# Kernel tuning notes

Measured on AMD Instinct MI355X. Metric: run time of the kernel, lower is better.

Reference implementation:

```python
import jax, jax.numpy as jnp
import numpy as np

B, T, H, L, OUT = 64, 2048, 256, 2, 256


def setup_inputs() -> dict:
    key = jax.random.key(0)
    ks = jax.random.split(key, 7)
    s = 1.0 / np.sqrt(H)
    return {
        "x": jax.random.normal(ks[0], (B, T, H), dtype=jnp.float32),
        "W_ih": jax.random.uniform(ks[1], (L, 4 * H, H), jnp.float32, -s, s),
        "W_hh": jax.random.uniform(ks[2], (L, 4 * H, H), jnp.float32, -s, s),
        "b_ih": jax.random.uniform(ks[3], (L, 4 * H), jnp.float32, -s, s),
        "b_hh": jax.random.uniform(ks[4], (L, 4 * H), jnp.float32, -s, s),
        "W_fc": jax.random.uniform(ks[5], (OUT, H), jnp.float32, -s, s),
        "b_fc": jax.random.uniform(ks[6], (OUT,), jnp.float32, -s, s),
    }


def _lstm_forward(x, W_ih, W_hh, b_ih, b_hh, W_fc, b_fc):
    n_layers = W_ih.shape[0]
    batch = x.shape[0]
    hidden = W_hh.shape[2]
    h0 = jnp.zeros((n_layers, batch, hidden), x.dtype)
    c0 = jnp.zeros((n_layers, batch, hidden), x.dtype)

    def step(carry, x_t):
        h, c = carry  # [L, B, H] each
        inp = x_t  # [B, in]
        new_h, new_c = [], []
        for l in range(n_layers):
            # gates: [B, 4H] = x W_ih^T + b_ih + h W_hh^T + b_hh
            gates = (inp @ W_ih[l].T + b_ih[l]) + (h[l] @ W_hh[l].T + b_hh[l])
            i_g, f_g, g_g, o_g = jnp.split(gates, 4, axis=-1)
            c_new = jax.nn.sigmoid(f_g) * c[l] + jax.nn.sigmoid(i_g) * jnp.tanh(g_g)
            h_new = jax.nn.sigmoid(o_g) * jnp.tanh(c_new)
            new_h.append(h_new)
            new_c.append(c_new)
            inp = h_new
        return (jnp.stack(new_h), jnp.stack(new_c)), None

    (h_T, _), _ = jax.lax.scan(step, (h0, c0), jnp.swapaxes(x, 0, 1))
    # fc applied to last timestep's top-layer hidden state
    return h_T[-1] @ W_fc.T + b_fc  # [B, OUT]


def reference(x, W_ih, W_hh, b_ih, b_hh, W_fc, b_fc):
    return _lstm_forward(x, W_ih, W_hh, b_ih, b_hh, W_fc, b_fc)
```

## Files before the change

### kernel.cpp

```cpp
#include <hip/hip_runtime.h>
#include <math.h>

typedef unsigned long long u64;
typedef __attribute__((ext_vector_type(8))) short short8v;
typedef __attribute__((ext_vector_type(4))) float f32x4;

#define LB 64
#define LT 2048
#define LH 256
#define LOUT 256
#define NWG 256

#define WS_CNT    0
#define WS_CNT_SZ ((size_t)8 * 32 * 16 * sizeof(int))
#define WS_H1     (64 * 1024)
#define WS_H2     (WS_H1 + 256 * 1024)
#define WS_BIAS   (WS_H2 + 256 * 1024)
#define WS_WT2    (1024 * 1024)
#define HSLOT     8192

#define MFMA(a, b, c) __builtin_amdgcn_mfma_f32_16x16x32_bf16(a, b, c, 0, 0, 0)
#define LD_IC(p) __hip_atomic_load((p), __ATOMIC_RELAXED, __HIP_MEMORY_SCOPE_AGENT)
#define ST_IC(p, v) __hip_atomic_store((p), (v), __ATOMIC_RELAXED, __HIP_MEMORY_SCOPE_AGENT)

__device__ __host__ __forceinline__ short bf16_rne(float f) {
    unsigned u = __builtin_bit_cast(unsigned, f);
    unsigned r = (u + 0x7fffu + ((u >> 16) & 1u)) >> 16;
    return (short)r;
}
__device__ __forceinline__ float bf16_to_f(short s) {
    unsigned u = ((unsigned)(unsigned short)s) << 16;
    return __builtin_bit_cast(float, u);
}
__device__ __forceinline__ float fsigm(float g) {
    return __builtin_amdgcn_rcpf(1.f + __builtin_amdgcn_exp2f(g * -1.44269504f));
}
__device__ __forceinline__ float ftanh(float g) {
    return __builtin_amdgcn_rcpf(1.f + __builtin_amdgcn_exp2f(g * -2.88539008f)) * 2.f - 1.f;
}

__global__ void prep_weights(const float* __restrict__ W_ih,
                             const float* __restrict__ W_hh,
                             const float* __restrict__ b_ih,
                             const float* __restrict__ b_hh,
                             unsigned short* __restrict__ Wt2,
                             float* __restrict__ bias_r) {
    int gid = blockIdx.x * 256 + threadIdx.x;
    if (gid >= (1 << 20)) return;
    int j   = gid & 7;
    int rwi = (gid >> 3) & 15;
    int kgi = (gid >> 7) & 3;
    int ks  = (gid >> 9) & 15;
    int mt  = (gid >> 13) & 3;
    int s   = (gid >> 15) & 15;
    int layer = gid >> 19;
    int k   = ks * 32 + kgi * 8 + j;
    int row = mt * 256 + s * 16 + rwi;
    float w = (k < 256) ? W_ih[((size_t)layer * 1024 + row) * 256 + k]
                        : W_hh[((size_t)layer * 1024 + row) * 256 + (k - 256)];
    short hi = bf16_rne(w);
    float rem = w - bf16_to_f(hi);
    short lo = bf16_rne(rem);
    size_t base = (((size_t)((layer * 16 + s) * 4 + mt) * 16 + ks) * 1024)
                  + (size_t)kgi * 128 + rwi * 8 + j;
    Wt2[base]       = (unsigned short)hi;
    Wt2[base + 512] = (unsigned short)lo;
    if (k == 0) {
        int ridx = s * 64 + mt * 16 + rwi;
        bias_r[layer * 1024 + ridx] = b_ih[layer * 1024 + row] + b_hh[layer * 1024 + row];
    }
}

__global__ __launch_bounds__(256, 1)
void lstm_persistent(const float* __restrict__ x,
                     const unsigned short* __restrict__ Wt2,
                     const float* __restrict__ bias_r,
                     u64* __restrict__ h1, u64* __restrict__ h2,
                     int* __restrict__ cnt)
{
    __shared__ __align__(16) f32x4 red[12][64];

    const int tid   = threadIdx.x;
    const int wg    = blockIdx.x;
    const int layer = wg >> 7;
    const int g     = wg & 127;
    const int bg    = g & 7;
    const int s     = g >> 3;
    const int b0    = bg * 8;
    const int wave  = tid >> 6;
    const int lane  = tid & 63;
    const int kg    = lane >> 4;
    const int rw    = lane & 15;
    const int rb    = rw & 7;
    const int batch = b0 + rb;
    int* const fl_base = cnt + (size_t)bg * 32 * 16;
    const int  myflag  = (layer * 16 + s) * 16;

    short8v Ahi[4][4], Alo[4][4];
    #pragma unroll
    for (int mt = 0; mt < 4; ++mt)
        #pragma unroll
        for (int k2 = 0; k2 < 4; ++k2) {
            size_t base = (((size_t)((layer * 16 + s) * 4 + mt) * 16 + (wave * 4 + k2)) * 1024)
                          + (size_t)kg * 128 + rw * 8;
            Ahi[mt][k2] = *(const short8v*)((const short*)Wt2 + base);
            Alo[mt][k2] = *(const short8v*)((const short*)Wt2 + base + 512);
        }

    f32x4 biasv[4];
    #pragma unroll
    for (int mt = 0; mt < 4; ++mt)
        biasv[mt] = *(const f32x4*)(bias_r + layer * 1024 + s * 64 + mt * 16 + kg * 4);

    f32x4 creg = {0.f, 0.f, 0.f, 0.f};

    float4 xr[4][2];
    if (layer == 0 && wave < 2) {
        #pragma unroll
        for (int k2 = 0; k2 < 4; ++k2) {
            const int kbase = (wave * 4 + k2) * 32 + kg * 8;
            const float* xp = x + ((size_t)batch * LT + 0) * LH + kbase;
            xr[k2][0] = *(const float4*)xp;
            xr[k2][1] = *(const float4*)(xp + 4);
        }
    }

    for (int r = 0; r <= LT; ++r) {
        const bool active = (layer == 0) ? (r < LT) : (r >= 1);
        const int t = (layer == 0) ? r : (r - 1);

        short8v Bhi[4], Blo[4];
        bool useB = false;
        if (active) {
            if (layer == 0 && wave < 2) {
                #pragma unroll
                for (int k2 = 0; k2 < 4; ++k2) {
                    float fv[8] = {xr[k2][0].x, xr[k2][0].y, xr[k2][0].z, xr[k2][0].w,
                                   xr[k2][1].x, xr[k2][1].y, xr[k2][1].z, xr[k2][1].w};
                    short8v bh, bl;
                    #pragma unroll
                    for (int j = 0; j < 8; ++j) {
                        short hb = bf16_rne(fv[j]);
                        bh[j] = hb;
                        bl[j] = bf16_rne(fv[j] - bf16_to_f(hb));
                    }
                    Bhi[k2] = bh; Blo[k2] = bl;
                }
                useB = true;
            } else {
                const u64* hb; size_t slotbase; int kofs; bool any;
                if (layer == 0) {
                    any = (t > 0); hb = h1; slotbase = (size_t)((t - 1) & 3) * HSLOT; kofs = -256;
                } else if (wave < 2) {
                    any = true;    hb = h1; slotbase = (size_t)(t & 3) * HSLOT; kofs = 0;
                } else {
                    any = (t > 0); hb = h2; slotbase = (size_t)((t - 1) & 3) * HSLOT; kofs = -256;
                }
                if (any) {
                    u64 q[4][4];
                    #pragma unroll
                    for (int k2 = 0; k2 < 4; ++k2) {
                        const int kbase = (wave * 4 + k2) * 32 + kg * 8 + kofs;
                        size_t qi = slotbase + (size_t)batch * 128 + (kbase >> 2) * 2;
                        q[k2][0] = LD_IC(hb + qi);
                        q[k2][1] = LD_IC(hb + qi + 1);
                        q[k2][2] = LD_IC(hb + qi + 2);
                        q[k2][3] = LD_IC(hb + qi + 3);
                    }
                    #pragma unroll
                    for (int k2 = 0; k2 < 4; ++k2) {
                        union { u64 qq[2]; short8v v; } ch, cl;
                        ch.qq[0] = q[k2][0]; ch.qq[1] = q[k2][2];
                        cl.qq[0] = q[k2][1]; cl.qq[1] = q[k2][3];
                        Bhi[k2] = ch.v; Blo[k2] = cl.v;
                    }
                    useB = true;
                }
            }
        }

        f32x4 acc[4];
        #pragma unroll
        for (int mt = 0; mt < 4; ++mt) acc[mt] = (f32x4){0.f, 0.f, 0.f, 0.f};
        if (useB) {
            #pragma unroll
            for (int k2 = 0; k2 < 4; ++k2)
                #pragma unroll
                for (int mt = 0; mt < 4; ++mt) {
                    acc[mt] = MFMA(Ahi[mt][k2], Bhi[k2], acc[mt]);
                    acc[mt] = MFMA(Ahi[mt][k2], Blo[k2], acc[mt]);
                    acc[mt] = MFMA(Alo[mt][k2], Bhi[k2], acc[mt]);
                }
        }

        if (active && wave > 0) {
            #pragma unroll
            for (int mt = 0; mt < 4; ++mt) red[(wave - 1) * 4 + mt][lane] = acc[mt];
        }
        __syncthreads();

        if (active && wave == 0) {
            f32x4 gate[4];
            #pragma unroll
            for (int mt = 0; mt < 4; ++mt) {
                f32x4 gs = acc[mt] + biasv[mt];
                #pragma unroll
                for (int w = 0; w < 3; ++w) gs += red[w * 4 + mt][lane];
                gate[mt] = gs;
            }
            float hv[4];
            #pragma unroll
            for (int rr = 0; rr < 4; ++rr) {
                float si = fsigm(gate[0][rr]);
                float sf = fsigm(gate[1][rr]);
                float so = fsigm(gate[3][rr]);
                float gg = ftanh(gate[2][rr]);
                float cn = sf * creg[rr] + si * gg;
                creg[rr] = cn;
                hv[rr] = so * ftanh(cn);
            }
            if (rw < 8) {
                u64 qh = 0, ql = 0;
                #pragma unroll
                for (int rr = 0; rr < 4; ++rr) {
                    short hb = bf16_rne(hv[rr]);
                    short lb = bf16_rne(hv[rr] - bf16_to_f(hb));
                    qh |= ((u64)(unsigned short)hb) << (16 * rr);
                    ql |= ((u64)(unsigned short)lb) << (16 * rr);
                }
                u64* dst = (layer == 0 ? h1 : h2);
                size_t qi = (size_t)(t & 3) * HSLOT + (size_t)(b0 + rw) * 128 + (s * 4 + kg) * 2;
                ST_IC(dst + qi, qh);
                ST_IC(dst + qi + 1, ql);
            }
        }

        if (wave == 0 && r < LT) {
            asm volatile("s_waitcnt vmcnt(0)" ::: "memory");
            if (lane == 0) ST_IC(fl_base + myflag, r + 1);
        }

        if (layer == 0 && wave < 2 && t + 1 < LT) {
            #pragma unroll
            for (int k2 = 0; k2 < 4; ++k2) {
                const int kbase = (wave * 4 + k2) * 32 + kg * 8;
                const float* xp = x + ((size_t)batch * LT + (t + 1)) * LH + kbase;
                xr[k2][0] = *(const float4*)xp;
                xr[k2][1] = *(const float4*)(xp + 4);
            }
        }

        if (r < LT) {
            if (wave == 0) {
                const int mL = lane >> 4;
                const int tgt = (layer == 0) ? ((mL == 0) ? r + 1 : r - 1) : (r + 1);
                const int* fp = fl_base + (size_t)(lane & 31) * 16;
                for (;;) {
                    int v = (lane < 32) ? LD_IC(fp) : 0x7fffffff;
                    if (__all(v >= tgt)) break;
                    __builtin_amdgcn_s_sleep(1);
                }
            }
            __syncthreads();
        }
    }
}

__global__ __launch_bounds__(256)
void fc_kernel(const u64* __restrict__ h2w,
               const float* __restrict__ W_fc,
               const float* __restrict__ b_fc,
               float* __restrict__ out) {
    int b = blockIdx.x;
    int o = threadIdx.x;
    __shared__ float hrow[LH];
    for (int k = threadIdx.x; k < LH; k += 256) {
        size_t w = (size_t)3 * HSLOT + (size_t)b * 128 + (k >> 2) * 2;
        int sh = (k & 3) * 16;
        short hi = (short)((h2w[w]     >> sh) & 0xffff);
        short lo = (short)((h2w[w + 1] >> sh) & 0xffff);
        hrow[k] = bf16_to_f(hi) + bf16_to_f(lo);
    }
    __syncthreads();
    float acc = b_fc[o];
#pragma unroll 8
    for (int k = 0; k < LH; ++k)
        acc = fmaf(W_fc[o * LH + k], hrow[k], acc);
    out[b * LOUT + o] = acc;
}

extern "C" void kernel_launch(void* const* d_in, const int* in_sizes, int n_in,
                              void* d_out, int out_size, void* d_ws, size_t ws_size,
                              hipStream_t stream) {
    const float* x    = (const float*)d_in[0];
    const float* W_ih = (const float*)d_in[1];
    const float* W_hh = (const float*)d_in[2];
    const float* b_ih = (const float*)d_in[3];
    const float* b_hh = (const float*)d_in[4];
    const float* W_fc = (const float*)d_in[5];
    const float* b_fc = (const float*)d_in[6];
    float* out = (float*)d_out;

    char* ws = (char*)d_ws;
    int*            cnt    = (int*)(ws + WS_CNT);
    u64*            h1     = (u64*)(ws + WS_H1);
    u64*            h2     = (u64*)(ws + WS_H2);
    float*          bias_r = (float*)(ws + WS_BIAS);
    unsigned short* Wt2    = (unsigned short*)(ws + WS_WT2);

    hipMemsetAsync(cnt, 0, WS_CNT_SZ, stream);
    prep_weights<<<(1 << 20) / 256, 256, 0, stream>>>(W_ih, W_hh, b_ih, b_hh, Wt2, bias_r);

    void* args[] = {(void*)&x, (void*)&Wt2, (void*)&bias_r,
                    (void*)&h1, (void*)&h2, (void*)&cnt};
    hipError_t e = hipLaunchCooperativeKernel(lstm_persistent, dim3(NWG), dim3(256),
                                              args, 0, stream);
    if (e != hipSuccess) {
        lstm_persistent<<<NWG, 256, 0, stream>>>(x, Wt2, bias_r, h1, h2, cnt);
    }

    fc_kernel<<<LB, 256, 0, stream>>>(h2, W_fc, b_fc, out);
}
```

Before: 8.513 ms.

## Embed parity tags in hidden-state data to replace flag-based inter-WG barriers

Removes the per-step flag barrier and __syncthreads wait. Consumers now poll the hidden-state data itself: a parity bit tied to the step is stored in the LSB of each low bf16 word, and data is written and read as 16-byte units with system-coherent loads and stores. Only a slim backpressure flag from layer 1 to layer 0 remains, and the LDS reduction buffer is double-buffered so consecutive steps do not race. This cuts synchronization latency on the recurrent critical path, at the cost of one bit of precision in the low correction term and relying on 16-byte store atomicity.

```diff
diff --git a/kernel.cpp b/kernel.cpp
--- a/kernel.cpp
+++ b/kernel.cpp
@@ -4,6 +4,7 @@
 typedef unsigned long long u64;
 typedef __attribute__((ext_vector_type(8))) short short8v;
 typedef __attribute__((ext_vector_type(4))) float f32x4;
+typedef __attribute__((ext_vector_type(4))) unsigned uint4v;
 
 #define LB 64
 #define LT 2048
@@ -12,12 +13,12 @@
 #define NWG 256
 
 #define WS_CNT    0
-#define WS_CNT_SZ ((size_t)8 * 32 * 16 * sizeof(int))
+#define WS_CNT_SZ ((size_t)8 * 16 * 16 * sizeof(int))
 #define WS_H1     (64 * 1024)
 #define WS_H2     (WS_H1 + 256 * 1024)
 #define WS_BIAS   (WS_H2 + 256 * 1024)
 #define WS_WT2    (1024 * 1024)
-#define HSLOT     8192
+#define HBYTES    (256 * 1024)
 
 #define MFMA(a, b, c) __builtin_amdgcn_mfma_f32_16x16x32_bf16(a, b, c, 0, 0, 0)
 #define LD_IC(p) __hip_atomic_load((p), __ATOMIC_RELAXED, __HIP_MEMORY_SCOPE_AGENT)
@@ -75,10 +76,10 @@
 void lstm_persistent(const float* __restrict__ x,
                      const unsigned short* __restrict__ Wt2,
                      const float* __restrict__ bias_r,
-                     u64* __restrict__ h1, u64* __restrict__ h2,
+                     char* __restrict__ h1c, char* __restrict__ h2c,
                      int* __restrict__ cnt)
 {
-    __shared__ __align__(16) f32x4 red[12][64];
+    __shared__ __align__(16) f32x4 red[2][12][64];
 
     const int tid   = threadIdx.x;
     const int wg    = blockIdx.x;
@@ -93,8 +94,7 @@
     const int rw    = lane & 15;
     const int rb    = rw & 7;
     const int batch = b0 + rb;
-    int* const fl_base = cnt + (size_t)bg * 32 * 16;
-    const int  myflag  = (layer * 16 + s) * 16;
+    int* const flags = cnt + bg * 256;
 
     short8v Ahi[4][4], Alo[4][4];
     #pragma unroll
@@ -148,32 +148,58 @@
                 }
                 useB = true;
             } else {
-                const u64* hb; size_t slotbase; int kofs; bool any;
-                if (layer == 0) {
-                    any = (t > 0); hb = h1; slotbase = (size_t)((t - 1) & 3) * HSLOT; kofs = -256;
-                } else if (wave < 2) {
-                    any = true;    hb = h1; slotbase = (size_t)(t & 3) * HSLOT; kofs = 0;
-                } else {
-                    any = (t > 0); hb = h2; slotbase = (size_t)((t - 1) & 3) * HSLOT; kofs = -256;
-                }
+                const char* hbuf; int slot, kofs, tg; bool any;
+                if (layer == 0)      { any = (t > 0); hbuf = h1c; slot = (t - 1) & 3; kofs = -256; tg = ((t - 1) >> 2) & 1; }
+                else if (wave < 2)   { any = true;    hbuf = h1c; slot = t & 3;       kofs = 0;    tg = (t >> 2) & 1; }
+                else                 { any = (t > 0); hbuf = h2c; slot = (t - 1) & 3; kofs = -256; tg = ((t - 1) >> 2) & 1; }
                 if (any) {
-                    u64 q[4][4];
-                    #pragma unroll
-                    for (int k2 = 0; k2 < 4; ++k2) {
-                        const int kbase = (wave * 4 + k2) * 32 + kg * 8 + kofs;
-                        size_t qi = slotbase + (size_t)batch * 128 + (kbase >> 2) * 2;
-                        q[k2][0] = LD_IC(hb + qi);
-                        q[k2][1] = LD_IC(hb + qi + 1);
-                        q[k2][2] = LD_IC(hb + qi + 2);
-                        q[k2][3] = LD_IC(hb + qi + 3);
+                    u64 a0, a1, a2, a3;
+                    {
+                        int hb0 = (wave * 4 + 0) * 32 + kg * 8 + kofs;
+                        int hb1 = hb0 + 32, hb2 = hb0 + 64, hb3 = hb0 + 96;
+                        a0 = (u64)(hbuf + (size_t)((((slot * 64 + batch) * 16) + (hb0 >> 4)) * 4 + ((hb0 >> 2) & 3)) * 16);
+                        a1 = (u64)(hbuf + (size_t)((((slot * 64 + batch) * 16) + (hb1 >> 4)) * 4 + ((hb1 >> 2) & 3)) * 16);
+                        a2 = (u64)(hbuf + (size_t)((((slot * 64 + batch) * 16) + (hb2 >> 4)) * 4 + ((hb2 >> 2) & 3)) * 16);
+                        a3 = (u64)(hbuf + (size_t)((((slot * 64 + batch) * 16) + (hb3 >> 4)) * 4 + ((hb3 >> 2) & 3)) * 16);
                     }
-                    #pragma unroll
-                    for (int k2 = 0; k2 < 4; ++k2) {
-                        union { u64 qq[2]; short8v v; } ch, cl;
-                        ch.qq[0] = q[k2][0]; ch.qq[1] = q[k2][2];
-                        cl.qq[0] = q[k2][1]; cl.qq[1] = q[k2][3];
-                        Bhi[k2] = ch.v; Blo[k2] = cl.v;
+                    const unsigned m = 0x00010001u;
+                    const unsigned wnt = tg ? 0x00010001u : 0u;
+                    uint4v U0, U1, U2, U3, U4, U5, U6, U7;
+                    for (;;) {
+                        asm volatile(
+                            "global_load_dwordx4 %0, %8, off sc0 sc1\n\t"
+                            "global_load_dwordx4 %1, %8, off offset:16 sc0 sc1\n\t"
+                            "global_load_dwordx4 %2, %9, off sc0 sc1\n\t"
+                            "global_load_dwordx4 %3, %9, off offset:16 sc0 sc1\n\t"
+                            "global_load_dwordx4 %4, %10, off sc0 sc1\n\t"
+                            "global_load_dwordx4 %5, %10, off offset:16 sc0 sc1\n\t"
+                            "global_load_dwordx4 %6, %11, off sc0 sc1\n\t"
+                            "global_load_dwordx4 %7, %11, off offset:16 sc0 sc1\n\t"
+                            "s_waitcnt vmcnt(0)"
+                            : "=v"(U0), "=v"(U1), "=v"(U2), "=v"(U3),
+                              "=v"(U4), "=v"(U5), "=v"(U6), "=v"(U7)
+                            : "v"(a0), "v"(a1), "v"(a2), "v"(a3)
+                            : "memory");
+                        unsigned bad = ((U0.z & m) ^ wnt) | ((U0.w & m) ^ wnt)
+                                     | ((U1.z & m) ^ wnt) | ((U1.w & m) ^ wnt)
+                                     | ((U2.z & m) ^ wnt) | ((U2.w & m) ^ wnt)
+                                     | ((U3.z & m) ^ wnt) | ((U3.w & m) ^ wnt)
+                                     | ((U4.z & m) ^ wnt) | ((U4.w & m) ^ wnt)
+                                     | ((U5.z & m) ^ wnt) | ((U5.w & m) ^ wnt)
+                                     | ((U6.z & m) ^ wnt) | ((U6.w & m) ^ wnt)
+                                     | ((U7.z & m) ^ wnt) | ((U7.w & m) ^ wnt);
+                        if (__all(bad == 0u)) break;
+                        __builtin_amdgcn_s_sleep(1);
                     }
+                    union { unsigned d[4]; short8v v; } bh, bl;
+                    bh.d[0] = U0.x; bh.d[1] = U0.y; bh.d[2] = U1.x; bh.d[3] = U1.y; Bhi[0] = bh.v;
+                    bl.d[0] = U0.z; bl.d[1] = U0.w; bl.d[2] = U1.z; bl.d[3] = U1.w; Blo[0] = bl.v;
+                    bh.d[0] = U2.x; bh.d[1] = U2.y; bh.d[2] = U3.x; bh.d[3] = U3.y; Bhi[1] = bh.v;
+                    bl.d[0] = U2.z; bl.d[1] = U2.w; bl.d[2] = U3.z; bl.d[3] = U3.w; Blo[1] = bl.v;
+                    bh.d[0] = U4.x; bh.d[1] = U4.y; bh.d[2] = U5.x; bh.d[3] = U5.y; Bhi[2] = bh.v;
+                    bl.d[0] = U4.z; bl.d[1] = U4.w; bl.d[2] = U5.z; bl.d[3] = U5.w; Blo[2] = bl.v;
+                    bh.d[0] = U6.x; bh.d[1] = U6.y; bh.d[2] = U7.x; bh.d[3] = U7.y; Bhi[3] = bh.v;
+                    bl.d[0] = U6.z; bl.d[1] = U6.w; bl.d[2] = U7.z; bl.d[3] = U7.w; Blo[3] = bl.v;
                     useB = true;
                 }
             }
@@ -195,9 +221,12 @@
 
         if (active && wave > 0) {
             #pragma unroll
-            for (int mt = 0; mt < 4; ++mt) red[(wave - 1) * 4 + mt][lane] = acc[mt];
+            for (int mt = 0; mt < 4; ++mt) red[r & 1][(wave - 1) * 4 + mt][lane] = acc[mt];
         }
         __syncthreads();
+
+        if (layer == 1 && wave == 0 && lane == 0)
+            ST_IC(flags + s * 16, r + 1);
 
         if (active && wave == 0) {
             f32x4 gate[4];
@@ -205,7 +234,7 @@
             for (int mt = 0; mt < 4; ++mt) {
                 f32x4 gs = acc[mt] + biasv[mt];
                 #pragma unroll
-                for (int w = 0; w < 3; ++w) gs += red[w * 4 + mt][lane];
+                for (int w = 0; w < 3; ++w) gs += red[r & 1][w * 4 + mt][lane];
                 gate[mt] = gs;
             }
             float hv[4];
@@ -219,25 +248,35 @@
                 creg[rr] = cn;
                 hv[rr] = so * ftanh(cn);
             }
+            if (layer == 0) {
+                const int tgt = r - 2;
+                const int* fp = flags + (lane & 15) * 16;
+                for (;;) {
+                    int v = (lane < 16) ? LD_IC(fp) : 0x7fffffff;
+                    if (__all(v >= tgt)) break;
+                    __builtin_amdgcn_s_sleep(1);
+                }
+            }
             if (rw < 8) {
+                const unsigned tgo = (unsigned)((t >> 2) & 1);
                 u64 qh = 0, ql = 0;
                 #pragma unroll
                 for (int rr = 0; rr < 4; ++rr) {
-                    short hb = bf16_rne(hv[rr]);
-                    short lb = bf16_rne(hv[rr] - bf16_to_f(hb));
-                    qh |= ((u64)(unsigned short)hb) << (16 * rr);
-                    ql |= ((u64)(unsigned short)lb) << (16 * rr);
-                }
-                u64* dst = (layer == 0 ? h1 : h2);
-                size_t qi = (size_t)(t & 3) * HSLOT + (size_t)(b0 + rw) * 128 + (s * 4 + kg) * 2;
-                ST_IC(dst + qi, qh);
-                ST_IC(dst + qi + 1, ql);
-            }
-        }
-
-        if (wave == 0 && r < LT) {
-            asm volatile("s_waitcnt vmcnt(0)" ::: "memory");
-            if (lane == 0) ST_IC(fl_base + myflag, r + 1);
+                    unsigned short hb = (unsigned short)bf16_rne(hv[rr]);
+                    unsigned short lb = (unsigned short)bf16_rne(hv[rr] - bf16_to_f((short)hb));
+                    lb = (unsigned short)((lb & ~1u) | tgo);
+                    qh |= ((u64)hb) << (16 * rr);
+                    ql |= ((u64)lb) << (16 * rr);
+                }
+                uint4v dd;
+                dd.x = (unsigned)qh; dd.y = (unsigned)(qh >> 32);
+                dd.z = (unsigned)ql; dd.w = (unsigned)(ql >> 32);
+                char* hbuf = (layer == 0 ? h1c : h2c);
+                int unit = (((t & 3) * 64 + (b0 + rw)) * 16 + s) * 4 + kg;
+                u64 ad = (u64)(hbuf + (size_t)unit * 16);
+                asm volatile("global_store_dwordx4 %0, %1, off sc0 sc1"
+                             :: "v"(ad), "v"(dd) : "memory");
+            }
         }
 
         if (layer == 0 && wave < 2 && t + 1 < LT) {
@@ -249,25 +288,11 @@
                 xr[k2][1] = *(const float4*)(xp + 4);
             }
         }
-
-        if (r < LT) {
-            if (wave == 0) {
-                const int mL = lane >> 4;
-                const int tgt = (layer == 0) ? ((mL == 0) ? r + 1 : r - 1) : (r + 1);
-                const int* fp = fl_base + (size_t)(lane & 31) * 16;
-                for (;;) {
-                    int v = (lane < 32) ? LD_IC(fp) : 0x7fffffff;
-                    if (__all(v >= tgt)) break;
-                    __builtin_amdgcn_s_sleep(1);
-                }
-            }
-            __syncthreads();
-        }
     }
 }
 
 __global__ __launch_bounds__(256)
-void fc_kernel(const u64* __restrict__ h2w,
+void fc_kernel(const char* __restrict__ h2c,
                const float* __restrict__ W_fc,
                const float* __restrict__ b_fc,
                float* __restrict__ out) {
@@ -275,11 +300,12 @@
     int o = threadIdx.x;
     __shared__ float hrow[LH];
     for (int k = threadIdx.x; k < LH; k += 256) {
-        size_t w = (size_t)3 * HSLOT + (size_t)b * 128 + (k >> 2) * 2;
+        int unit = ((3 * 64 + b) * 16 + (k >> 4)) * 4 + ((k >> 2) & 3);
+        const u64* up = (const u64*)(h2c + (size_t)unit * 16);
+        u64 qh = up[0];
+        u64 ql = up[1] & ~0x0001000100010001ULL;
         int sh = (k & 3) * 16;
-        short hi = (short)((h2w[w]     >> sh) & 0xffff);
-        short lo = (short)((h2w[w + 1] >> sh) & 0xffff);
-        hrow[k] = bf16_to_f(hi) + bf16_to_f(lo);
+        hrow[k] = bf16_to_f((short)(qh >> sh)) + bf16_to_f((short)(ql >> sh));
     }
     __syncthreads();
     float acc = b_fc[o];
@@ -303,21 +329,23 @@
 
     char* ws = (char*)d_ws;
     int*            cnt    = (int*)(ws + WS_CNT);
-    u64*            h1     = (u64*)(ws + WS_H1);
-    u64*            h2     = (u64*)(ws + WS_H2);
+    char*           h1c    = ws + WS_H1;
+    char*           h2c    = ws + WS_H2;
     float*          bias_r = (float*)(ws + WS_BIAS);
     unsigned short* Wt2    = (unsigned short*)(ws + WS_WT2);
 
     hipMemsetAsync(cnt, 0, WS_CNT_SZ, stream);
+    hipMemsetAsync(h1c, 0xFF, HBYTES, stream);
+    hipMemsetAsync(h2c, 0xFF, HBYTES, stream);
     prep_weights<<<(1 << 20) / 256, 256, 0, stream>>>(W_ih, W_hh, b_ih, b_hh, Wt2, bias_r);
 
     void* args[] = {(void*)&x, (void*)&Wt2, (void*)&bias_r,
-                    (void*)&h1, (void*)&h2, (void*)&cnt};
+                    (void*)&h1c, (void*)&h2c, (void*)&cnt};
     hipError_t e = hipLaunchCooperativeKernel(lstm_persistent, dim3(NWG), dim3(256),
                                               args, 0, stream);
     if (e != hipSuccess) {
-        lstm_persistent<<<NWG, 256, 0, stream>>>(x, Wt2, bias_r, h1, h2, cnt);
-    }
-
-    fc_kernel<<<LB, 256, 0, stream>>>(h2, W_fc, b_fc, out);
-}
+        lstm_persistent<<<NWG, 256, 0, stream>>>(x, Wt2, bias_r, h1c, h2c, cnt);
+    }
+
+    fc_kernel<<<LB, 256, 0, stream>>>(h2c, W_fc, b_fc, out);
+}
```

Result: slower. 9.317 ms (+9.4%).
